# Kernel optimization log

Hardware: AMD Instinct MI355X
Metric: run time of the kernel (lower is better)

The kernel has to match this reference:

```python
import jax, jax.numpy as jnp
import numpy as np

B, S, DIM, HDIM = 8, 1024, 1024, 128
H = DIM // HDIM  # 8 heads
GN_EPS = 1e-3    # keras GroupNormalization default epsilon


def group_norm(y, gamma, beta, groups, eps=GN_EPS):
    # keras GroupNormalization on [B,S,C]: reshape to [B,S,groups,C//groups],
    # normalize over all axes except batch and group axis -> axes (1,3).
    b, s, c = y.shape
    g = y.reshape(b, s, groups, c // groups)
    mean = g.mean(axis=(1, 3), keepdims=True)
    var = g.var(axis=(1, 3), keepdims=True)
    g = (g - mean) * jax.lax.rsqrt(var + eps)
    return g.reshape(b, s, c) * gamma + beta


def setup_inputs() -> dict:
    key = jax.random.key(0)
    ks = jax.random.split(key, 7)
    x = jax.random.normal(ks[0], (B, S, DIM), dtype=jnp.float32)
    sc_h = 1.0 / np.sqrt(HDIM).astype(np.float32)
    sc_d = 1.0 / np.sqrt(DIM).astype(np.float32)
    Wq = jax.random.normal(ks[1], (H, HDIM, HDIM), dtype=jnp.float32) * sc_h
    Wk = jax.random.normal(ks[2], (H, HDIM, HDIM), dtype=jnp.float32) * sc_h
    Wv = jax.random.normal(ks[3], (H, HDIM, HDIM), dtype=jnp.float32) * sc_h
    Wg = jax.random.normal(ks[4], (DIM, DIM), dtype=jnp.float32) * sc_d
    Wo = jax.random.normal(ks[5], (DIM, DIM), dtype=jnp.float32) * sc_d
    gn_gamma = jnp.ones((DIM,), dtype=jnp.float32)
    gn_beta = jnp.zeros((DIM,), dtype=jnp.float32)
    return {"x": x, "Wq": Wq, "Wk": Wk, "Wv": Wv, "Wg": Wg, "Wo": Wo,
            "gn_gamma": gn_gamma, "gn_beta": gn_beta}


def reference(x, Wq, Wk, Wv, Wg, Wo, gn_gamma, gn_beta):
    b, s, c = x.shape
    h, hd = Wq.shape[0], Wq.shape[1]
    # gating branch: W = ReLU(x @ Wg)
    Wgate = jax.nn.relu(jnp.einsum('bsc,cd->bsd', x, Wg))
    # split channels into heads: [B,S,H,hd]
    xh = x.reshape(b, s, h, hd)
    Q = jnp.einsum('bshd,hde->bhse', xh, Wq)
    K = jnp.einsum('bshd,hde->bhse', xh, Wk)
    V = jnp.einsum('bshd,hde->bhse', xh, Wv)
    # per-head decay mask D[h,i,j] = gamma_h ** (i - j) (full, non-causal as in source)
    idx = jnp.arange(s, dtype=jnp.float32)
    gammas = 1.0 - 2.0 ** (-5.0 - jnp.arange(h, dtype=jnp.float32))  # [H]
    decay = gammas[:, None, None] ** (idx[None, :, None] - idx[None, None, :])  # [H,S,S]
    scores = jnp.einsum('bhsd,bhtd->bhst', Q, K) * decay[None]
    ret = jnp.einsum('bhst,bhtd->bhsd', scores, V)       # [B,H,S,hd]
    y = ret.transpose(0, 2, 1, 3).reshape(b, s, c)        # concat heads
    Y = group_norm(y, gn_gamma, gn_beta, groups=hd)       # groups = hdim (keras arg)
    return jnp.einsum('bsc,cd->bsd', Wgate * Y, Wo)
```

## Files before the change

### kernel.cpp

```cpp
#include <hip/hip_runtime.h>

#define BB 8
#define SS 1024
#define DD 1024
#define HH 8
#define HD 128
#define GN_EPS 1e-3f

typedef __attribute__((ext_vector_type(8))) short bf16x8;
typedef __attribute__((ext_vector_type(4))) float f32x4;

__device__ __forceinline__ short f2bf(float f) {
    unsigned u = __float_as_uint(f);
    return (short)((u + 0x7fffu + ((u >> 16) & 1u)) >> 16);
}
__device__ __forceinline__ float bf2f(short s) {
    return __uint_as_float(((unsigned)(unsigned short)s) << 16);
}

__device__ __forceinline__ void gload16(const void* g, void* l) {
    __builtin_amdgcn_global_load_lds((const __attribute__((address_space(1))) void*)g,
                                     (__attribute__((address_space(3))) void*)l, 16, 0, 0);
}

__device__ __forceinline__ void stage_tile(const short* __restrict__ G, size_t ld, int k0,
                                           short* lds, int wid, int lane) {
#pragma unroll
    for (int i = 0; i < 2; i++) {
        const int seg = wid * 2 + i;
        const int row = seg * 8 + (lane >> 3);
        const int chunk = (lane & 7) ^ (lane >> 3);
        gload16(G + (size_t)row * ld + k0 + chunk * 8, lds + seg * 512);
    }
}

__device__ __forceinline__ void gemm_tile_g(
    const short* __restrict__ A, size_t ldA,
    const short* __restrict__ B, size_t ldB,
    int K, short* As, short* Bs, f32x4 acc[4][2])
{
    const int tid = threadIdx.x, lane = tid & 63, wid = tid >> 6;
    const int wr = (wid >> 2) * 64, wc = (wid & 3) * 32;
    const int fr = lane & 15, fc = lane >> 4;
    const int rsw = fr & 7;
#pragma unroll
    for (int i = 0; i < 4; i++)
#pragma unroll
        for (int j = 0; j < 2; j++) acc[i][j] = (f32x4){0.f, 0.f, 0.f, 0.f};

    const int nt = K >> 6;
    stage_tile(A, ldA, 0, As, wid, lane);
    stage_tile(B, ldB, 0, Bs, wid, lane);
    if (nt > 1) {
        stage_tile(A, ldA, 64, As + 8192, wid, lane);
        stage_tile(B, ldB, 64, Bs + 8192, wid, lane);
    }
    for (int t = 0; t < nt; t++) {
        if (t + 1 < nt) asm volatile("s_waitcnt vmcnt(4)" ::: "memory");
        else            asm volatile("s_waitcnt vmcnt(0)" ::: "memory");
        __builtin_amdgcn_s_barrier();
        __builtin_amdgcn_sched_barrier(0);
        const int cur = t & 1;
        const short* as = As + (cur << 13);
        const short* bs = Bs + (cur << 13);
#pragma unroll
        for (int half = 0; half < 2; half++) {
            const int slot = ((half * 4 + fc) ^ rsw) << 3;
            bf16x8 af[4], bfv[2];
#pragma unroll
            for (int i = 0; i < 4; i++) af[i] = *(const bf16x8*)&as[(wr + i * 16 + fr) * 64 + slot];
#pragma unroll
            for (int j = 0; j < 2; j++) bfv[j] = *(const bf16x8*)&bs[(wc + j * 16 + fr) * 64 + slot];
#pragma unroll
            for (int i = 0; i < 4; i++)
#pragma unroll
                for (int j = 0; j < 2; j++)
                    acc[i][j] = __builtin_amdgcn_mfma_f32_16x16x32_bf16(af[i], bfv[j], acc[i][j], 0, 0, 0);
        }
        __builtin_amdgcn_sched_barrier(0);
        asm volatile("s_waitcnt lgkmcnt(0)" ::: "memory");
        __builtin_amdgcn_s_barrier();
        if (t + 2 < nt) {
            stage_tile(A, ldA, (t + 2) << 6, As + (cur << 13), wid, lane);
            stage_tile(B, ldB, (t + 2) << 6, Bs + (cur << 13), wid, lane);
        }
    }
}

__global__ __launch_bounds__(256) void prep(
    const float* __restrict__ x,
    const float* __restrict__ Wq, const float* __restrict__ Wk, const float* __restrict__ Wv,
    const float* __restrict__ Wg, const float* __restrict__ Wo,
    short* __restrict__ xb, short* __restrict__ WgT, short* __restrict__ WoT,
    short* __restrict__ Wt, float* __restrict__ sQ, float* __restrict__ sK,
    float* __restrict__ Sp)
{
    __shared__ float t[32][33];
    int bid = blockIdx.x;
    const int tid = threadIdx.x;
    if (bid < 4096) {
        const size_t i = ((size_t)bid * 256 + tid) * 8;
        float4 a = *(const float4*)&x[i];
        float4 b = *(const float4*)&x[i + 4];
        bf16x8 v;
        v[0] = f2bf(a.x); v[1] = f2bf(a.y); v[2] = f2bf(a.z); v[3] = f2bf(a.w);
        v[4] = f2bf(b.x); v[5] = f2bf(b.y); v[6] = f2bf(b.z); v[7] = f2bf(b.w);
        *(bf16x8*)&xb[i] = v;
        return;
    }
    bid -= 4096;
    if (bid < 2048) {
        const float* __restrict__ S = (bid < 1024) ? Wg : Wo;
        short* __restrict__ D = (bid < 1024) ? WgT : WoT;
        const int tb = bid & 1023;
        const int bx = (tb & 31) * 32, by = (tb >> 5) * 32;
        const int xx = tid & 31, y0 = tid >> 5;
#pragma unroll
        for (int r = 0; r < 32; r += 8) t[y0 + r][xx] = S[(size_t)(by + y0 + r) * 1024 + bx + xx];
        __syncthreads();
#pragma unroll
        for (int r = 0; r < 32; r += 8) D[(size_t)(bx + y0 + r) * 1024 + by + xx] = f2bf(t[xx][y0 + r]);
        return;
    }
    bid -= 2048;
    if (bid < 384) {
        const int ht = bid >> 4, tb = bid & 15;
        const int typ = ht >> 3, h = ht & 7;
        const float* __restrict__ W = (typ == 0 ? Wq : (typ == 1 ? Wk : Wv)) + (size_t)h * HD * HD;
        short* __restrict__ D = Wt + (size_t)ht * HD * HD;
        const int bx = (tb & 3) * 32, by = (tb >> 2) * 32;
        const int xx = tid & 31, y0 = tid >> 5;
#pragma unroll
        for (int r = 0; r < 32; r += 8) t[y0 + r][xx] = W[(by + y0 + r) * HD + bx + xx];
        __syncthreads();
#pragma unroll
        for (int r = 0; r < 32; r += 8) D[(bx + y0 + r) * HD + by + xx] = f2bf(t[xx][y0 + r]);
        return;
    }
    bid -= 384;
    if (bid < 32) {
        const int h = bid >> 2;
        const int s = (bid & 3) * 256 + tid;
        const double gamma = 1.0 - exp2((double)(-5 - h));
        const double lg = log2(gamma);
        sQ[h * SS + s] = (float)exp2(lg * (double)s);
        sK[h * SS + s] = (float)exp2(-lg * (double)s);
        return;
    }
    *(float4*)&Sp[tid * 8] = (float4){0.f, 0.f, 0.f, 0.f};
    *(float4*)&Sp[tid * 8 + 4] = (float4){0.f, 0.f, 0.f, 0.f};
}

__global__ __launch_bounds__(512) void g_qkvgate(
    const short* __restrict__ xb, const short* __restrict__ Wt, const short* __restrict__ WgT,
    const float* __restrict__ sQ, const float* __restrict__ sK,
    short* __restrict__ Qb, short* __restrict__ Ktb, short* __restrict__ Vtb,
    short* __restrict__ gateb)
{
    __shared__ short As[2 * 8192], Bs[2 * 8192];
    f32x4 acc[4][2];
    const int orig = blockIdx.x;
    const int cx = orig & 7, p = orig >> 3;
    const int tid = threadIdx.x, lane = tid & 63, wid = tid >> 6;
    const int wr = (wid >> 2) * 64, wc = (wid & 3) * 32;
    const int r0 = (lane >> 4) * 4, c = lane & 15;

    if (p < 64) {
        const int w2 = cx * 64 + p;
        const int m0 = (w2 >> 3) * 128, n0 = (w2 & 7) * 128;
        gemm_tile_g(xb + (size_t)m0 * DD, DD, WgT + (size_t)n0 * DD, DD, DD, As, Bs, acc);
#pragma unroll
        for (int i = 0; i < 4; i++)
#pragma unroll
            for (int j = 0; j < 2; j++)
#pragma unroll
                for (int r = 0; r < 4; r++)
                    gateb[(size_t)(m0 + wr + i * 16 + r0 + r) * DD + n0 + wc + j * 16 + c] =
                        f2bf(fmaxf(acc[i][j][r], 0.f));
        return;
    }
    const int w = cx * 64 + (p - 64);
    const int mt = w >> 3, h = w & 7;
    const int m0 = mt * 128;
    const int b = m0 >> 10, s0 = m0 & (SS - 1);
    const int bh = (b << 3) + h;
    const short* __restrict__ A = xb + (size_t)m0 * DD + h * HD;

    const int fr = lane & 15, fc = lane >> 4;
    const int rsw = fr & 7;

    stage_tile(A, DD, 0,  As,        wid, lane);
    stage_tile(A, DD, 64, As + 8192, wid, lane);
    stage_tile(Wt + (size_t)h * HD * HD, HD, 0, Bs, wid, lane);
    __syncthreads();

#pragma unroll
    for (int i = 0; i < 4; i++)
#pragma unroll
        for (int j = 0; j < 2; j++) acc[i][j] = (f32x4){0.f, 0.f, 0.f, 0.f};

    int sb = 0;
    for (int st = 0; st < 6; st++) {
        if (st + 1 < 6) {
            const int typn = (st + 1) >> 1, ktn = (st + 1) & 1;
            stage_tile(Wt + (size_t)(typn * 8 + h) * HD * HD, HD, ktn * 64,
                       Bs + ((sb ^ 1) << 13), wid, lane);
        }
        const int kt = st & 1;
        const short* as = As + (kt << 13);
        const short* bs = Bs + (sb << 13);
#pragma unroll
        for (int half = 0; half < 2; half++) {
            const int slot = ((half * 4 + fc) ^ rsw) << 3;
            bf16x8 af[4], bfv[2];
#pragma unroll
            for (int i = 0; i < 4; i++) af[i] = *(const bf16x8*)&as[(wr + i * 16 + fr) * 64 + slot];
#pragma unroll
            for (int j = 0; j < 2; j++) bfv[j] = *(const bf16x8*)&bs[(wc + j * 16 + fr) * 64 + slot];
#pragma unroll
            for (int i = 0; i < 4; i++)
#pragma unroll
                for (int j = 0; j < 2; j++)
                    acc[i][j] = __builtin_amdgcn_mfma_f32_16x16x32_bf16(af[i], bfv[j], acc[i][j], 0, 0, 0);
        }
        __syncthreads();
        sb ^= 1;
        if (kt == 1) {
            const int typ = st >> 1;
            if (typ == 0) {
#pragma unroll
                for (int i = 0; i < 4; i++)
#pragma unroll
                    for (int j = 0; j < 2; j++)
#pragma unroll
                        for (int r = 0; r < 4; r++) {
                            const int s = s0 + wr + i * 16 + r0 + r;
                            Qb[((size_t)bh * SS + s) * HD + wc + j * 16 + c] =
                                f2bf(acc[i][j][r] * sQ[h * SS + s]);
                        }
            } else if (typ == 1) {
                short* __restrict__ Ob = Ktb + (size_t)bh * HD * SS;
#pragma unroll
                for (int i = 0; i < 4; i++)
#pragma unroll
                    for (int j = 0; j < 2; j++) {
                        const int tb = s0 + wr + i * 16 + r0;
                        const int d = wc + j * 16 + c;
                        short4 o;
                        o.x = f2bf(acc[i][j][0] * sK[h * SS + tb + 0]);
                        o.y = f2bf(acc[i][j][1] * sK[h * SS + tb + 1]);
                        o.z = f2bf(acc[i][j][2] * sK[h * SS + tb + 2]);
                        o.w = f2bf(acc[i][j][3] * sK[h * SS + tb + 3]);
                        *(short4*)&Ob[(size_t)d * SS + tb] = o;
                    }
            } else {
                short* __restrict__ Ob = Vtb + (size_t)bh * HD * SS;
#pragma unroll
                for (int i = 0; i < 4; i++)
#pragma unroll
                    for (int j = 0; j < 2; j++) {
                        const int tb = s0 + wr + i * 16 + r0;
                        const int e = wc + j * 16 + c;
                        short4 o;
                        o.x = f2bf(acc[i][j][0]); o.y = f2bf(acc[i][j][1]);
                        o.z = f2bf(acc[i][j][2]); o.w = f2bf(acc[i][j][3]);
                        *(short4*)&Ob[(size_t)e * SS + tb] = o;
                    }
            }
#pragma unroll
            for (int i = 0; i < 4; i++)
#pragma unroll
                for (int j = 0; j < 2; j++) acc[i][j] = (f32x4){0.f, 0.f, 0.f, 0.f};
        }
    }
}

__global__ __launch_bounds__(512) void g_kv(
    const short* __restrict__ Vtb, const short* __restrict__ Ktb, float* __restrict__ Mp)
{
    __shared__ short As[2 * 8192], Bs[2 * 8192];
    f32x4 acc[4][2];
    const int orig = blockIdx.x;
    const int w = (orig & 7) * 32 + (orig >> 3);
    const int chunk = w & 3, bh = w >> 2;
    gemm_tile_g(Vtb + (size_t)bh * HD * SS + chunk * 256, SS,
                Ktb + (size_t)bh * HD * SS + chunk * 256, SS, 256, As, Bs, acc);
    const int tid = threadIdx.x, lane = tid & 63, wid = tid >> 6;
    const int wr = (wid >> 2) * 64, wc = (wid & 3) * 32;
    const int r0 = (lane >> 4) * 4, c = lane & 15;
    float* __restrict__ Ob = Mp + (size_t)w * HD * HD;
#pragma unroll
    for (int i = 0; i < 4; i++)
#pragma unroll
        for (int j = 0; j < 2; j++)
#pragma unroll
            for (int r = 0; r < 4; r++)
                Ob[(size_t)(wr + i * 16 + r0 + r) * HD + wc + j * 16 + c] = acc[i][j][r];
}

__global__ __launch_bounds__(256) void g_mredcvt(const float* __restrict__ Mp, short* __restrict__ Mtb) {
    const size_t i = ((size_t)blockIdx.x * 256 + threadIdx.x) * 8;
    const size_t bh = i >> 14, ij = i & 16383;
    const float* p = Mp + (bh * 4) * 16384 + ij;
    float s[8];
#pragma unroll
    for (int q = 0; q < 8; q++) s[q] = 0.f;
#pragma unroll
    for (int cth = 0; cth < 4; cth++) {
        float4 a = *(const float4*)&p[cth * 16384];
        float4 b = *(const float4*)&p[cth * 16384 + 4];
        s[0] += a.x; s[1] += a.y; s[2] += a.z; s[3] += a.w;
        s[4] += b.x; s[5] += b.y; s[6] += b.z; s[7] += b.w;
    }
    bf16x8 v;
#pragma unroll
    for (int q = 0; q < 8; q++) v[q] = f2bf(s[q]);
    *(bf16x8*)&Mtb[i] = v;
}

__global__ __launch_bounds__(512) void g_qm(
    const short* __restrict__ Qb, const short* __restrict__ Mtb,
    short* __restrict__ retc, float* __restrict__ Sp)
{
    __shared__ short As[2 * 8192], Bs[2 * 8192];
    f32x4 acc[4][2];
    const int orig = blockIdx.x;
    const int w = (orig & 7) * 64 + (orig >> 3);
    const int bh = w >> 3, m0 = (w & 7) * 128;
    gemm_tile_g(Qb + ((size_t)bh * SS + m0) * HD, HD,
                Mtb + (size_t)bh * HD * HD, HD, HD, As, Bs, acc);
    const int tid = threadIdx.x, lane = tid & 63, wid = tid >> 6;
    const int wr = (wid >> 2) * 64, wc = (wid & 3) * 32;
    const int r0 = (lane >> 4) * 4, c = lane & 15;
    const int b_ = bh >> 3, h_ = bh & 7;
    short* __restrict__ O = retc + ((size_t)(b_ * SS + m0)) * DD + h_ * HD;
#pragma unroll
    for (int i = 0; i < 4; i++)
#pragma unroll
        for (int j = 0; j < 2; j++)
#pragma unroll
            for (int r = 0; r < 4; r++)
                O[(size_t)(wr + i * 16 + r0 + r) * DD + wc + j * 16 + c] = f2bf(acc[i][j][r]);

    float psm[2], psq[2];
#pragma unroll
    for (int j = 0; j < 2; j++) { psm[j] = 0.f; psq[j] = 0.f; }
#pragma unroll
    for (int i = 0; i < 4; i++)
#pragma unroll
        for (int j = 0; j < 2; j++)
#pragma unroll
            for (int r = 0; r < 4; r++) {
                const float v = acc[i][j][r];
                psm[j] += v; psq[j] += v * v;
            }
    const int masks[5] = {1, 2, 4, 16, 32};
#pragma unroll
    for (int mk = 0; mk < 5; mk++) {
#pragma unroll
        for (int j = 0; j < 2; j++) {
            psm[j] += __shfl_xor(psm[j], masks[mk], 64);
            psq[j] += __shfl_xor(psq[j], masks[mk], 64);
        }
    }
    if ((lane & 7) == 0 && lane < 16) {
        const int hi = lane >> 3;
#pragma unroll
        for (int j = 0; j < 2; j++) {
            const int g = b_ * 128 + h_ * 16 + (wid & 3) * 4 + j * 2 + hi;
            atomicAdd(&Sp[g * 2 + 0], psm[j]);
            atomicAdd(&Sp[g * 2 + 1], psq[j]);
        }
    }
}

__global__ __launch_bounds__(256) void aprep(
    const short* __restrict__ gateb, const short* __restrict__ retc,
    const float* __restrict__ Sp,
    const float* __restrict__ gng, const float* __restrict__ gnb, short* __restrict__ Ab)
{
    const size_t idx = ((size_t)blockIdx.x * 256 + threadIdx.x) * 4;
    const int m = (int)(idx >> 10), cc = (int)(idx & 1023);
    const int b_ = m >> 10, g = b_ * 128 + (cc >> 3);
    const float sm = Sp[g * 2 + 0], sq = Sp[g * 2 + 1];
    const float mu = sm * (1.0f / 8192.0f);
    float var = sq * (1.0f / 8192.0f) - mu * mu;
    if (var < 0.f) var = 0.f;
    const float rs = rsqrtf(var + GN_EPS);
    short4 gv4 = *(const short4*)&gateb[idx];
    short4 rv4 = *(const short4*)&retc[idx];
    float4 gv = *(const float4*)&gng[cc];
    float4 bv = *(const float4*)&gnb[cc];
    short4 o;
    o.x = f2bf(bf2f(gv4.x) * ((bf2f(rv4.x) - mu) * rs * gv.x + bv.x));
    o.y = f2bf(bf2f(gv4.y) * ((bf2f(rv4.y) - mu) * rs * gv.y + bv.y));
    o.z = f2bf(bf2f(gv4.z) * ((bf2f(rv4.z) - mu) * rs * gv.z + bv.z));
    o.w = f2bf(bf2f(gv4.w) * ((bf2f(rv4.w) - mu) * rs * gv.w + bv.w));
    *(short4*)&Ab[idx] = o;
}

__global__ __launch_bounds__(512) void g_final(
    const short* __restrict__ Ab, const short* __restrict__ WoT, float* __restrict__ out)
{
    __shared__ short As[2 * 8192], Bs[2 * 8192];
    f32x4 acc[4][2];
    const int orig = blockIdx.x;
    const int w = (orig & 7) * 64 + (orig >> 3);
    const int m0 = (w >> 3) * 128, n0 = (w & 7) * 128;
    gemm_tile_g(Ab + (size_t)m0 * DD, DD, WoT + (size_t)n0 * DD, DD, DD, As, Bs, acc);
    const int tid = threadIdx.x, lane = tid & 63, wid = tid >> 6;
    const int wr = (wid >> 2) * 64, wc = (wid & 3) * 32;
    const int r0 = (lane >> 4) * 4, c = lane & 15;
#pragma unroll
    for (int i = 0; i < 4; i++)
#pragma unroll
        for (int j = 0; j < 2; j++)
#pragma unroll
            for (int r = 0; r < 4; r++)
                out[(size_t)(m0 + wr + i * 16 + r0 + r) * DD + n0 + wc + j * 16 + c] = acc[i][j][r];
}

extern "C" void kernel_launch(void* const* d_in, const int* in_sizes, int n_in,
                              void* d_out, int out_size, void* d_ws, size_t ws_size,
                              hipStream_t stream)
{
    const float* x   = (const float*)d_in[0];
    const float* Wq  = (const float*)d_in[1];
    const float* Wk  = (const float*)d_in[2];
    const float* Wv  = (const float*)d_in[3];
    const float* Wg  = (const float*)d_in[4];
    const float* Wo  = (const float*)d_in[5];
    const float* gng = (const float*)d_in[6];
    const float* gnb = (const float*)d_in[7];
    float* out = (float*)d_out;

    char* ws = (char*)d_ws;
    size_t off = 0;
    auto alloc = [&](size_t bytes) -> void* {
        void* p = ws + off;
        off += (bytes + 255) & ~(size_t)255;
        return p;
    };
    const size_t NE = (size_t)BB * SS * DD;
    float*  sQ    = (float*)alloc((size_t)HH * SS * sizeof(float));
    float*  sK    = (float*)alloc((size_t)HH * SS * sizeof(float));
    short*  xb    = (short*)alloc(NE * sizeof(short));
    short*  WgT   = (short*)alloc((size_t)DD * DD * sizeof(short));
    short*  WoT   = (short*)alloc((size_t)DD * DD * sizeof(short));
    short*  Wt    = (short*)alloc((size_t)24 * HD * HD * sizeof(short));
    short*  Qb    = (short*)alloc(NE * sizeof(short));
    short*  Ktb   = (short*)alloc(NE * sizeof(short));
    short*  Vtb   = (short*)alloc(NE * sizeof(short));
    short*  retc  = (short*)alloc(NE * sizeof(short));
    short*  gateb = (short*)alloc(NE * sizeof(short));
    short*  Ab    = (short*)alloc(NE * sizeof(short));
    float*  Mp    = (float*)alloc((size_t)256 * HD * HD * sizeof(float));
    short*  Mtb   = (short*)alloc((size_t)64 * HD * HD * sizeof(short));
    float*  Sp    = (float*)alloc((size_t)1024 * 2 * sizeof(float));

    prep<<<dim3(6561), 256, 0, stream>>>(x, Wq, Wk, Wv, Wg, Wo, xb, WgT, WoT, Wt, sQ, sK, Sp);
    g_qkvgate<<<dim3(1024), 512, 0, stream>>>(xb, Wt, WgT, sQ, sK, Qb, Ktb, Vtb, gateb);
    g_kv<<<dim3(256), 512, 0, stream>>>(Vtb, Ktb, Mp);
    g_mredcvt<<<dim3(512), 256, 0, stream>>>(Mp, Mtb);
    g_qm<<<dim3(512), 512, 0, stream>>>(Qb, Mtb, retc, Sp);
    aprep<<<dim3(8192), 256, 0, stream>>>(gateb, retc, Sp, gng, gnb, Ab);
    g_final<<<dim3(512), 512, 0, stream>>>(Ab, WoT, out);
}
```

Measured before the change: 113.6 us.

## Halve KV split-K chunks and specialize QM GEMM with single-shot staging

The K^T V reduction now uses two 512-long chunks per batch-head instead of four 256-long chunks. That halves the partial-sum buffer, the g_kv grid size and the reduction reads in g_mredcvt. The g_qm kernel no longer calls the generic pipelined gemm_tile_g: it stages both 64-wide K tiles of Q and M into LDS up front, waits once, and runs the MFMA loop with no per-iteration synchronisation. The cost is that only 128 blocks run for g_kv, which lowers parallelism on a chip with many CUs.

```diff
diff --git a/kernel.cpp b/kernel.cpp
--- a/kernel.cpp
+++ b/kernel.cpp
@@ -281,10 +281,10 @@
     __shared__ short As[2 * 8192], Bs[2 * 8192];
     f32x4 acc[4][2];
     const int orig = blockIdx.x;
-    const int w = (orig & 7) * 32 + (orig >> 3);
-    const int chunk = w & 3, bh = w >> 2;
-    gemm_tile_g(Vtb + (size_t)bh * HD * SS + chunk * 256, SS,
-                Ktb + (size_t)bh * HD * SS + chunk * 256, SS, 256, As, Bs, acc);
+    const int w = (orig & 7) * 16 + (orig >> 3);
+    const int chunk = w & 1, bh = w >> 1;
+    gemm_tile_g(Vtb + (size_t)bh * HD * SS + chunk * 512, SS,
+                Ktb + (size_t)bh * HD * SS + chunk * 512, SS, 512, As, Bs, acc);
     const int tid = threadIdx.x, lane = tid & 63, wid = tid >> 6;
     const int wr = (wid >> 2) * 64, wc = (wid & 3) * 32;
     const int r0 = (lane >> 4) * 4, c = lane & 15;
@@ -301,12 +301,12 @@
 __global__ __launch_bounds__(256) void g_mredcvt(const float* __restrict__ Mp, short* __restrict__ Mtb) {
     const size_t i = ((size_t)blockIdx.x * 256 + threadIdx.x) * 8;
     const size_t bh = i >> 14, ij = i & 16383;
-    const float* p = Mp + (bh * 4) * 16384 + ij;
+    const float* p = Mp + (bh * 2) * 16384 + ij;
     float s[8];
 #pragma unroll
     for (int q = 0; q < 8; q++) s[q] = 0.f;
 #pragma unroll
-    for (int cth = 0; cth < 4; cth++) {
+    for (int cth = 0; cth < 2; cth++) {
         float4 a = *(const float4*)&p[cth * 16384];
         float4 b = *(const float4*)&p[cth * 16384 + 4];
         s[0] += a.x; s[1] += a.y; s[2] += a.z; s[3] += a.w;
@@ -327,11 +327,43 @@
     const int orig = blockIdx.x;
     const int w = (orig & 7) * 64 + (orig >> 3);
     const int bh = w >> 3, m0 = (w & 7) * 128;
-    gemm_tile_g(Qb + ((size_t)bh * SS + m0) * HD, HD,
-                Mtb + (size_t)bh * HD * HD, HD, HD, As, Bs, acc);
+    const short* __restrict__ A = Qb + ((size_t)bh * SS + m0) * HD;
+    const short* __restrict__ Bp = Mtb + (size_t)bh * HD * HD;
     const int tid = threadIdx.x, lane = tid & 63, wid = tid >> 6;
     const int wr = (wid >> 2) * 64, wc = (wid & 3) * 32;
+    const int fr = lane & 15, fc = lane >> 4, rsw = fr & 7;
     const int r0 = (lane >> 4) * 4, c = lane & 15;
+
+    stage_tile(A,  HD, 0,  As,        wid, lane);
+    stage_tile(A,  HD, 64, As + 8192, wid, lane);
+    stage_tile(Bp, HD, 0,  Bs,        wid, lane);
+    stage_tile(Bp, HD, 64, Bs + 8192, wid, lane);
+#pragma unroll
+    for (int i = 0; i < 4; i++)
+#pragma unroll
+        for (int j = 0; j < 2; j++) acc[i][j] = (f32x4){0.f, 0.f, 0.f, 0.f};
+    asm volatile("s_waitcnt vmcnt(0)" ::: "memory");
+    __builtin_amdgcn_s_barrier();
+    __builtin_amdgcn_sched_barrier(0);
+#pragma unroll
+    for (int kt = 0; kt < 2; kt++) {
+        const short* as = As + (kt << 13);
+        const short* bs = Bs + (kt << 13);
+#pragma unroll
+        for (int half = 0; half < 2; half++) {
+            const int slot = ((half * 4 + fc) ^ rsw) << 3;
+            bf16x8 af[4], bfv[2];
+#pragma unroll
+            for (int i = 0; i < 4; i++) af[i] = *(const bf16x8*)&as[(wr + i * 16 + fr) * 64 + slot];
+#pragma unroll
+            for (int j = 0; j < 2; j++) bfv[j] = *(const bf16x8*)&bs[(wc + j * 16 + fr) * 64 + slot];
+#pragma unroll
+            for (int i = 0; i < 4; i++)
+#pragma unroll
+                for (int j = 0; j < 2; j++)
+                    acc[i][j] = __builtin_amdgcn_mfma_f32_16x16x32_bf16(af[i], bfv[j], acc[i][j], 0, 0, 0);
+        }
+    }
     const int b_ = bh >> 3, h_ = bh & 7;
     short* __restrict__ O = retc + ((size_t)(b_ * SS + m0)) * DD + h_ * HD;
 #pragma unroll
@@ -454,13 +486,13 @@
     short*  retc  = (short*)alloc(NE * sizeof(short));
     short*  gateb = (short*)alloc(NE * sizeof(short));
     short*  Ab    = (short*)alloc(NE * sizeof(short));
-    float*  Mp    = (float*)alloc((size_t)256 * HD * HD * sizeof(float));
+    float*  Mp    = (float*)alloc((size_t)128 * HD * HD * sizeof(float));
     short*  Mtb   = (short*)alloc((size_t)64 * HD * HD * sizeof(short));
     float*  Sp    = (float*)alloc((size_t)1024 * 2 * sizeof(float));
 
     prep<<<dim3(6561), 256, 0, stream>>>(x, Wq, Wk, Wv, Wg, Wo, xb, WgT, WoT, Wt, sQ, sK, Sp);
     g_qkvgate<<<dim3(1024), 512, 0, stream>>>(xb, Wt, WgT, sQ, sK, Qb, Ktb, Vtb, gateb);
-    g_kv<<<dim3(256), 512, 0, stream>>>(Vtb, Ktb, Mp);
+    g_kv<<<dim3(128), 512, 0, stream>>>(Vtb, Ktb, Mp);
     g_mredcvt<<<dim3(512), 256, 0, stream>>>(Mp, Mtb);
     g_qm<<<dim3(512), 512, 0, stream>>>(Qb, Mtb, retc, Sp);
     aprep<<<dim3(8192), 256, 0, stream>>>(gateb, retc, Sp, gng, gnb, Ab);
```

Result: no change. 112.3 us (-1.1%).
